# Performance work log

Measured on AMD Instinct MI355X. Metric: run time of the kernel, lower is better.

## Reference

```python
import jax, jax.numpy as jnp
import numpy as np

Nc, Nd, Ns = 8000, 6000, 6000          # circRNA / drug / disease node counts
F, H, O = 64, 4, 64                    # feature dim (fcir=fdrug=fdis), GAT heads, cnn out_channels
Ec, Ed, Es = 256000, 192000, 192000    # directed edge counts per graph
NEG_SLOPE = 0.2


def _gcn(x, src, dst, ew, W, b, N):
    # PyG GCNConv w/ edge_weight: add self loops (w=1), symmetric norm, x@W.T, scatter-add
    loop = jnp.arange(N, dtype=src.dtype)
    s = jnp.concatenate([src, loop])
    d = jnp.concatenate([dst, loop])
    w = jnp.concatenate([ew, jnp.ones((N,), x.dtype)])
    deg = jax.ops.segment_sum(w, d, num_segments=N)
    dinv = jnp.where(deg > 0, jax.lax.rsqrt(deg), 0.0)
    norm = dinv[s] * w * dinv[d]                        # [E+N]
    h = x @ W.T                                         # [N,F]
    return jax.ops.segment_sum(h[s] * norm[:, None], d, num_segments=N) + b


def _gat(x, src, dst, ew, W, a_src, a_dst, We, a_edge, b, N):
    # PyG GATConv(heads=H, concat=False, edge_dim=1); self loops with fill_value='mean'
    E = src.shape[0]
    ea = ew[:, None]                                    # [E,1]
    cnt = jax.ops.segment_sum(jnp.ones((E,), x.dtype), dst, num_segments=N)
    esum = jax.ops.segment_sum(ea, dst, num_segments=N)
    loop_attr = esum / jnp.maximum(cnt, 1.0)[:, None]   # per-dst mean edge attr
    loop = jnp.arange(N, dtype=src.dtype)
    s = jnp.concatenate([src, loop])
    d = jnp.concatenate([dst, loop])
    ea = jnp.concatenate([ea, loop_attr], axis=0)       # [E+N,1]
    h = (x @ W.T).reshape(N, H, F)
    al_s = jnp.einsum('nhf,hf->nh', h, a_src)
    al_d = jnp.einsum('nhf,hf->nh', h, a_dst)
    e = (ea @ We.T).reshape(-1, H, F)
    al_e = jnp.einsum('ehf,hf->eh', e, a_edge)
    alpha = al_s[s] + al_d[d] + al_e                    # [E+N,H]
    alpha = jnp.where(alpha >= 0, alpha, NEG_SLOPE * alpha)   # leaky_relu
    amax = jax.ops.segment_max(alpha, d, num_segments=N)
    ex = jnp.exp(alpha - amax[d])
    denom = jax.ops.segment_sum(ex, d, num_segments=N)
    coef = ex / denom[d]                                # segment softmax over incoming edges
    out = jax.ops.segment_sum(h[s] * coef[:, :, None], d, num_segments=N)  # [N,H,F]
    return out.mean(axis=1) + b                         # concat=False -> head mean


def _readout(x1, x2, W, b):
    # Conv1d(in=2, out=O, kernel=(F,1)) on [1,2,F,N] == full contraction over (layer, feature)
    X = jnp.stack([x1, x2], axis=0)                     # [2,N,F]
    return jnp.einsum('cnf,ocf->no', X, W) + b          # [N,O]


def _forward(fl, cir_edges, drug_edges, dis_edges):
    def branch(x, ei, ew, g1W, g1b, gaW, gas, gad, gaeW, gae, gab, g2W, g2b, N):
        src, dst = ei[0], ei[1]
        f1 = jax.nn.relu(_gcn(x, src, dst, ew, g1W, g1b, N))
        att = jax.nn.relu(_gat(f1, src, dst, ew, gaW, gas, gad, gaeW, gae, gab, N))
        f2 = jax.nn.relu(_gcn(att, src, dst, ew, g2W, g2b, N))
        return f1, f2

    cf1, cf2 = branch(fl['x_cir'], cir_edges, fl['cir_ew'], fl['gcn_cir1_W'], fl['gcn_cir1_b'],
                      fl['gat_cir_W'], fl['gat_cir_asrc'], fl['gat_cir_adst'], fl['gat_cir_eW'],
                      fl['gat_cir_aedge'], fl['gat_cir_b'], fl['gcn_cir2_W'], fl['gcn_cir2_b'], Nc)
    # NOTE: the source forward reuses the *_dis GCN/GAT layers for the drug branch (faithful)
    df1, df2 = branch(fl['x_drug'], drug_edges, fl['drug_ew'], fl['gcn_dis1_W'], fl['gcn_dis1_b'],
                      fl['gat_dis_W'], fl['gat_dis_asrc'], fl['gat_dis_adst'], fl['gat_dis_eW'],
                      fl['gat_dis_aedge'], fl['gat_dis_b'], fl['gcn_dis2_W'], fl['gcn_dis2_b'], Nd)
    sf1, sf2 = branch(fl['x_dis'], dis_edges, fl['dis_ew'], fl['gcn_dis1_W'], fl['gcn_dis1_b'],
                      fl['gat_dis_W'], fl['gat_dis_asrc'], fl['gat_dis_adst'], fl['gat_dis_eW'],
                      fl['gat_dis_aedge'], fl['gat_dis_b'], fl['gcn_dis2_W'], fl['gcn_dis2_b'], Ns)
    cir_fea = _readout(cf1, cf2, fl['cnn_cir_W'], fl['cnn_cir_b'])
    drug_fea = _readout(df1, df2, fl['cnn_dis_W'], fl['cnn_dis_b'])   # source uses cnn_dis for drug too
    dis_fea = _readout(sf1, sf2, fl['cnn_dis_W'], fl['cnn_dis_b'])
    return (cir_fea @ dis_fea.T, cir_fea @ drug_fea.T, drug_fea @ dis_fea.T,
            cir_fea, drug_fea, dis_fea)


_PARAM_SHAPES = [
    ('gcn_cir1_W', (F, F)), ('gcn_cir1_b', (F,)),
    ('gcn_cir2_W', (F, F)), ('gcn_cir2_b', (F,)),
    ('gcn_dis1_W', (F, F)), ('gcn_dis1_b', (F,)),
    ('gcn_dis2_W', (F, F)), ('gcn_dis2_b', (F,)),
    ('gat_cir_W', (H * F, F)), ('gat_cir_asrc', (H, F)), ('gat_cir_adst', (H, F)),
    ('gat_cir_eW', (H * F, 1)), ('gat_cir_aedge', (H, F)), ('gat_cir_b', (F,)),
    ('gat_dis_W', (H * F, F)), ('gat_dis_asrc', (H, F)), ('gat_dis_adst', (H, F)),
    ('gat_dis_eW', (H * F, 1)), ('gat_dis_aedge', (H, F)), ('gat_dis_b', (F,)),
    ('cnn_cir_W', (O, 2, F)), ('cnn_cir_b', (O,)),
    ('cnn_dis_W', (O, 2, F)), ('cnn_dis_b', (O,)),
]


def setup_inputs() -> dict:
    key = jax.random.key(0)
    ks = iter(jax.random.split(key, 64))
    inp = {}
    inp['x_cir'] = jax.random.normal(next(ks), (Nc, F), jnp.float32)
    inp['x_drug'] = jax.random.normal(next(ks), (Nd, F), jnp.float32)
    inp['x_dis'] = jax.random.normal(next(ks), (Ns, F), jnp.float32)
    inp['cir_edges'] = jax.random.randint(next(ks), (2, Ec), 0, Nc, dtype=jnp.int32)
    inp['cir_ew'] = jax.random.uniform(next(ks), (Ec,), jnp.float32)
    inp['drug_edges'] = jax.random.randint(next(ks), (2, Ed), 0, Nd, dtype=jnp.int32)
    inp['drug_ew'] = jax.random.uniform(next(ks), (Ed,), jnp.float32)
    inp['dis_edges'] = jax.random.randint(next(ks), (2, Es), 0, Ns, dtype=jnp.int32)
    inp['dis_ew'] = jax.random.uniform(next(ks), (Es,), jnp.float32)
    for name, shape in _PARAM_SHAPES:
        inp[name] = jax.random.normal(next(ks), shape, jnp.float32) * 0.1
    return inp


def reference(x_cir, x_drug, x_dis, cir_edges, cir_ew, drug_edges, drug_ew, dis_edges, dis_ew,
              gcn_cir1_W, gcn_cir1_b, gcn_cir2_W, gcn_cir2_b,
              gcn_dis1_W, gcn_dis1_b, gcn_dis2_W, gcn_dis2_b,
              gat_cir_W, gat_cir_asrc, gat_cir_adst, gat_cir_eW, gat_cir_aedge, gat_cir_b,
              gat_dis_W, gat_dis_asrc, gat_dis_adst, gat_dis_eW, gat_dis_aedge, gat_dis_b,
              cnn_cir_W, cnn_cir_b, cnn_dis_W, cnn_dis_b):
    fl = {k: v for k, v in locals().items() if k not in ('cir_edges', 'drug_edges', 'dis_edges')}
    return _forward(fl, cir_edges, drug_edges, dis_edges)
```

## Files before the change

### kernel.cpp

```cpp
#include <hip/hip_runtime.h>

#define NEG_SLOPE 0.2f

typedef __attribute__((ext_vector_type(8))) short bfrag;
typedef __attribute__((ext_vector_type(4))) float f32x4;

static __device__ __forceinline__ ushort f2bf(float x){
  uint u = __float_as_uint(x);
  uint r = (u + 0x7fff + ((u>>16)&1)) >> 16;
  return (ushort)r;
}
static __device__ __forceinline__ float bf2f(ushort h){
  return __uint_as_float(((uint)h)<<16);
}
static __device__ __forceinline__ float rdlane(float v, int l){
  return __int_as_float(__builtin_amdgcn_readlane(__float_as_int(v), l));
}


struct G3 {
  const int* src[3]; const int* dst[3]; const float* ew[3];
  float* deg[3]; int* cnt[3]; int* pos[3];
  float* dinv[3]; float* lat[3]; int* rowp[3];
  int4* ep[3];
  int N[3]; int E[3];
};

struct MM3 {
  const float* A[3]; const float* B[3]; float* C[3]; const float* bias[3];
  ushort* H[3]; ushort* L[3];
  const float* gas[3]; const float* gad[3];
  float* als[3]; float* ald[3];
  int M[3]; int lda, ldb, N2;
};

struct AGG3 {
  const float* h[3]; const float* dinv[3]; const int* rowp[3];
  const int4* ep[3]; const float* bias[3];
  float* out[3]; int N[3]; int ostride, ooff;
};

struct GAT3 {
  const float* hg[3]; const float* als[3]; const float* ald[3];
  const float* lat[3]; const float* ce[3]; const int* rowp[3];
  const int4* ep[3]; const float* bias[3];
  float* out[3]; int N[3];
};

struct SC3 {
  const ushort* AH[3]; const ushort* AL[3];
  const ushort* BH[3]; const ushort* BL[3];
  float* C[3]; int M[3]; int N2;
};


__global__ void k_edge_stats_b(G3 g){
  int b = blockIdx.z;
  int e = blockIdx.x*blockDim.x + threadIdx.x;
  if (e < g.E[b]){
    int d = g.dst[b][e];
    atomicAdd(&g.deg[b][d], g.ew[b][e]);
    atomicAdd(&g.cnt[b][d], 1);
  }
}

__global__ void k_scan_b(G3 g, const float* gaeW_c, const float* gae_c, float* ce_c,
                         const float* gaeW_d, const float* gae_d, float* ce_d){
  int b = blockIdx.x;
  int tid = threadIdx.x;
  if (b < 2 && tid < 64){
    const float* W = b ? gaeW_d : gaeW_c;
    const float* Aa = b ? gae_d : gae_c;
    float* ceo = b ? ce_d : ce_c;
    #pragma unroll
    for (int hh=0; hh<4; hh++){
      float v = W[hh*64+tid] * Aa[hh*64+tid];
      #pragma unroll
      for (int off=32; off>0; off>>=1) v += __shfl_down(v,off);
      if (tid==0) ceo[hh] = v;
    }
  }
  int N = g.N[b];
  const float* deg = g.deg[b];
  const int* cnt = g.cnt[b];
  float* dinv = g.dinv[b];
  float* lat = g.lat[b];
  int* rowp = g.rowp[b];
  const int T = 1024, PER = 8;
  __shared__ int ssum[T];
  int base = tid*PER;
  int loc[PER]; int s = 0;
  #pragma unroll
  for (int u=0;u<PER;u++){
    int i = base+u;
    int c = (i<N)? cnt[i] : 0;
    loc[u] = s; s += c;
    if (i<N){
      float d = deg[i];
      dinv[i] = rsqrtf(d);
      lat[i] = (d - 1.0f) / fmaxf((float)c, 1.0f);
    }
  }
  ssum[tid] = s; __syncthreads();
  for (int off=1; off<T; off<<=1){
    int t = (tid>=off)? ssum[tid-off] : 0;
    __syncthreads();
    ssum[tid] += t;
    __syncthreads();
  }
  int excl = ssum[tid] - s;
  #pragma unroll
  for (int u=0;u<PER;u++){ int i=base+u; if (i<N) rowp[i] = excl + loc[u]; }
  if (tid == T-1) rowp[N] = ssum[T-1];
}

__global__ void k_scatter_b(G3 g){
  int b = blockIdx.z;
  int e = blockIdx.x*blockDim.x + threadIdx.x;
  if (e < g.E[b]){
    int d = g.dst[b][e];
    int s = g.src[b][e];
    float w = g.ew[b][e];
    float dw = g.dinv[b][s] * w;
    int p = g.rowp[b][d] + atomicAdd(&g.pos[b][d], 1);
    g.ep[b][p] = make_int4(s, __float_as_int(w), __float_as_int(dw), 0);
  }
}


template<int K, bool BIAS, bool SPLIT, bool ALQ, bool INIT>
__global__ __launch_bounds__(256)
void k_mm_b(MM3 P, G3 g){
  if (INIT && blockIdx.x == gridDim.x-1){
    int b = blockIdx.z;
    int i = blockIdx.y*256 + threadIdx.x;
    if (i < g.N[b]){ g.deg[b][i] = 1.0f; g.cnt[b][i] = 0; g.pos[b][i] = 0; }
    return;
  }
  int br = blockIdx.z;
  int M = P.M[br];
  int bi = blockIdx.y*128;
  if (bi >= M) return;
  int N2 = P.N2;
  int bj = blockIdx.x*128;
  const float* __restrict__ A = P.A[br];
  const float* __restrict__ B = P.B[br];
  float* __restrict__ C = P.C[br];
  int lda = P.lda, ldb = P.ldb;

  __shared__ float As[128*36];
  __shared__ float Bs[32*132];
  int tid = threadIdx.x;
  int tx = tid & 15, ty = tid >> 4;
  float acc[8][8] = {};

  for (int kh = 0; kh < K; kh += 32){
    for (int t = tid; t < 1024; t += 256){
      int r = t >> 3, k4 = (t & 7) << 2;
      int gr = bi + r;
      float4 v = (gr < M) ? *(const float4*)(A + (size_t)gr*lda + kh + k4)
                          : make_float4(0.f,0.f,0.f,0.f);
      *(float4*)(As + r*36 + k4) = v;
    }
    for (int t = tid; t < 1024; t += 256){
      int r = t >> 3, k4 = (t & 7) << 2;
      int gr = bj + r;
      float4 v = (gr < N2) ? *(const float4*)(B + (size_t)gr*ldb + kh + k4)
                           : make_float4(0.f,0.f,0.f,0.f);
      Bs[(k4+0)*132 + r] = v.x;
      Bs[(k4+1)*132 + r] = v.y;
      Bs[(k4+2)*132 + r] = v.z;
      Bs[(k4+3)*132 + r] = v.w;
    }
    __syncthreads();
    #pragma unroll
    for (int k = 0; k < 32; k += 4){
      float4 a4[8];
      #pragma unroll
      for (int u=0; u<4; u++){
        a4[u]   = *(const float4*)(As + (ty*4+u)*36 + k);
        a4[u+4] = *(const float4*)(As + (64+ty*4+u)*36 + k);
      }
      #pragma unroll
      for (int i=0; i<4; i++){
        float4 bl = *(const float4*)(Bs + (k+i)*132 + tx*4);
        float4 bh = *(const float4*)(Bs + (k+i)*132 + 64 + tx*4);
        #pragma unroll
        for (int u=0; u<8; u++){
          float av = (i==0)?a4[u].x : (i==1)?a4[u].y : (i==2)?a4[u].z : a4[u].w;
          acc[u][0] += av*bl.x; acc[u][1] += av*bl.y;
          acc[u][2] += av*bl.z; acc[u][3] += av*bl.w;
          acc[u][4] += av*bh.x; acc[u][5] += av*bh.y;
          acc[u][6] += av*bh.z; acc[u][7] += av*bh.w;
        }
      }
    }
    __syncthreads();
  }

  #pragma unroll
  for (int u=0; u<8; u++){
    int gi = bi + ((u<4) ? (ty*4+u) : (64+ty*4+(u-4)));
    if (gi >= M) continue;
    #pragma unroll
    for (int half=0; half<2; half++){
      int gj = bj + ((half==0) ? tx*4 : 64+tx*4);
      int v0 = half*4;
      if (gj + 4 <= N2){
        float4 r4 = make_float4(acc[u][v0],acc[u][v0+1],acc[u][v0+2],acc[u][v0+3]);
        if (BIAS){
          const float* bb = P.bias[br];
          r4.x += bb[gj]; r4.y += bb[gj+1]; r4.z += bb[gj+2]; r4.w += bb[gj+3];
        }
        *(float4*)(C + (size_t)gi*N2 + gj) = r4;
        if (SPLIT){
          ushort hv[4], lv[4];
          float vv[4] = {r4.x, r4.y, r4.z, r4.w};
          #pragma unroll
          for (int v=0; v<4; v++){
            hv[v] = f2bf(vv[v]);
            lv[v] = f2bf(vv[v] - bf2f(hv[v]));
          }
          *(ushort4*)(P.H[br] + (size_t)gi*N2 + gj) = make_ushort4(hv[0],hv[1],hv[2],hv[3]);
          *(ushort4*)(P.L[br] + (size_t)gi*N2 + gj) = make_ushort4(lv[0],lv[1],lv[2],lv[3]);
        }
      } else {
        for (int v=0; v<4; v++) if (gj+v < N2){
          float r = acc[u][v0+v];
          if (BIAS) r += P.bias[br][gj+v];
          C[(size_t)gi*N2+gj+v] = r;
        }
      }
    }
  }

  if (ALQ){
    int h0 = bj >> 6;
    float ps[8][2], pd[8][2];
    #pragma unroll
    for (int u=0;u<8;u++){ ps[u][0]=0.f; ps[u][1]=0.f; pd[u][0]=0.f; pd[u][1]=0.f; }
    #pragma unroll
    for (int half=0; half<2; half++){
      #pragma unroll
      for (int v=0; v<4; v++){
        int cw = tx*4 + v;
        float gs = P.gas[br][(h0+half)*64 + cw];
        float gd = P.gad[br][(h0+half)*64 + cw];
        #pragma unroll
        for (int u=0;u<8;u++){
          ps[u][half] += acc[u][half*4+v]*gs;
          pd[u][half] += acc[u][half*4+v]*gd;
        }
      }
    }
    #pragma unroll
    for (int u=0;u<8;u++){
      #pragma unroll
      for (int hf=0; hf<2; hf++){
        float s = ps[u][hf], d = pd[u][hf];
        #pragma unroll
        for (int off=8; off>0; off>>=1){ s += __shfl_down(s,off); d += __shfl_down(d,off); }
        if (tx==0){
          int gi = bi + ((u<4) ? (ty*4+u) : (64+ty*4+(u-4)));
          if (gi < M){
            P.als[br][gi*4 + h0 + hf] = s;
            P.ald[br][gi*4 + h0 + hf] = d;
          }
        }
      }
    }
  }
}


__global__ void k_gcn_agg_b(AGG3 P){
  int b = blockIdx.z;
  int wid = (blockIdx.x*blockDim.x + threadIdx.x) >> 6;
  int f = threadIdx.x & 63;
  if (wid >= P.N[b]) return;
  const float* __restrict__ h = P.h[b];
  const int4* __restrict__ ep = P.ep[b];
  float dn = P.dinv[b][wid];
  float acc = dn*h[(size_t)wid*64 + f];
  int p0 = P.rowp[b][wid], p1 = P.rowp[b][wid+1];
  for (int p=p0; p<p1; p++){
    int4 pr = ep[p];
    acc = fmaf(__int_as_float(pr.z), h[(size_t)pr.x*64 + f], acc);
  }
  P.out[b][(size_t)wid*P.ostride + P.ooff + f] = fmaxf(fmaf(dn, acc, P.bias[b][f]), 0.f);
}


__global__ void k_gat_agg_b(GAT3 P){
  int b = blockIdx.z;
  int wid = (blockIdx.x*blockDim.x + threadIdx.x) >> 6;
  int lane = threadIdx.x & 63;
  if (wid >= P.N[b]) return;
  const float* __restrict__ hg = P.hg[b];
  const float* __restrict__ als = P.als[b];
  const int4* __restrict__ ep = P.ep[b];
  int h = lane & 3;
  int el = lane >> 2;
  int f = lane;

  float4 cv = *(const float4*)P.ce[b];
  float4 adv = *(const float4*)(P.ald[b] + (size_t)wid*4);
  float4 asv = *(const float4*)(als + (size_t)wid*4);
  float c_l  = (h==0)?cv.x :(h==1)?cv.y :(h==2)?cv.z :cv.w;
  float ad_l = (h==0)?adv.x:(h==1)?adv.y:(h==2)?adv.z:adv.w;
  float as_l = (h==0)?asv.x:(h==1)?asv.y:(h==2)?asv.z:asv.w;
  float la = P.lat[b][wid];

  float a_self = as_l + ad_l + la*c_l;
  a_self = (a_self >= 0.f) ? a_self : NEG_SLOPE*a_self;
  float m = a_self;

  int p0 = P.rowp[b][wid], p1 = P.rowp[b][wid+1];

  for (int c0=p0; c0<p1; c0+=16){
    int idx = c0 + el;
    float a = -1e30f;
    if (idx < p1){
      int4 pr = ep[idx];
      float w = __int_as_float(pr.y);
      a = als[pr.x*4 + h] + ad_l + w*c_l;
      a = (a >= 0.f) ? a : NEG_SLOPE*a;
    }
    #pragma unroll
    for (int off=4; off<64; off<<=1) a = fmaxf(a, __shfl_xor(a, off));
    m = fmaxf(m, a);
  }

  float ex_self = __expf(a_self - m);
  float l = ex_self;
  const float* hn = hg + (size_t)wid*256;
  float acc0 = rdlane(ex_self,0) * hn[f];
  float acc1 = rdlane(ex_self,1) * hn[64+f];
  float acc2 = rdlane(ex_self,2) * hn[128+f];
  float acc3 = rdlane(ex_self,3) * hn[192+f];

  for (int c0=p0; c0<p1; c0+=16){
    int idx = c0 + el;
    float ex = 0.f;
    int s_lane = 0;
    if (idx < p1){
      int4 pr = ep[idx];
      s_lane = pr.x;
      float w = __int_as_float(pr.y);
      float a = als[s_lane*4 + h] + ad_l + w*c_l;
      a = (a >= 0.f) ? a : NEG_SLOPE*a;
      ex = __expf(a - m);
    }
    float ls = ex;
    #pragma unroll
    for (int off=4; off<64; off<<=1) ls += __shfl_xor(ls, off);
    l += ls;
    int cnt = p1 - c0; if (cnt > 16) cnt = 16;
    for (int e=0; e<cnt; e++){
      int s = __builtin_amdgcn_readlane(s_lane, e*4);
      const float* hs = hg + (size_t)s*256 + f;
      float x0 = rdlane(ex, e*4+0);
      float x1 = rdlane(ex, e*4+1);
      float x2 = rdlane(ex, e*4+2);
      float x3 = rdlane(ex, e*4+3);
      acc0 = fmaf(x0, hs[0],   acc0);
      acc1 = fmaf(x1, hs[64],  acc1);
      acc2 = fmaf(x2, hs[128], acc2);
      acc3 = fmaf(x3, hs[192], acc3);
    }
  }
  float o = acc0/rdlane(l,0) + acc1/rdlane(l,1) + acc2/rdlane(l,2) + acc3/rdlane(l,3);
  P.out[b][(size_t)wid*64 + f] = fmaxf(0.25f*o + P.bias[b][f], 0.f);
}


__global__ __launch_bounds__(256)
void k_score(SC3 P){
  int br = blockIdx.z;
  int M = P.M[br];
  int bi = blockIdx.y*128;
  if (bi >= M) return;
  int N = P.N2;
  int bj = blockIdx.x*128;
  const ushort* __restrict__ AH = P.AH[br];
  const ushort* __restrict__ ALo = P.AL[br];
  const ushort* __restrict__ BH = P.BH[br];
  const ushort* __restrict__ BLo = P.BL[br];
  float* __restrict__ C = P.C[br];

  int wv = threadIdx.x >> 6;
  int lane = threadIdx.x & 63;
  int la = lane & 15, lk = lane >> 4;
  int r0 = bi + (wv>>1)*64;
  int c0 = bj + (wv&1)*64;

  bfrag ah[4][2], al[4][2];
  #pragma unroll
  for (int mi=0; mi<4; mi++){
    int r = r0 + mi*16 + la; if (r > M-1) r = M-1;
    size_t base = (size_t)r*64 + lk*8;
    ah[mi][0] = *(const bfrag*)(AH + base);
    ah[mi][1] = *(const bfrag*)(AH + base + 32);
    al[mi][0] = *(const bfrag*)(ALo + base);
    al[mi][1] = *(const bfrag*)(ALo + base + 32);
  }

  f32x4 acc[4][4];
  #pragma unroll
  for (int mi=0; mi<4; mi++)
    #pragma unroll
    for (int ni=0; ni<4; ni++)
      acc[mi][ni] = (f32x4){0.f,0.f,0.f,0.f};

  #pragma unroll
  for (int ni=0; ni<4; ni++){
    int cc = c0 + ni*16 + la; if (cc > N-1) cc = N-1;
    size_t base = (size_t)cc*64 + lk*8;
    bfrag bh0 = *(const bfrag*)(BH + base);
    bfrag bh1 = *(const bfrag*)(BH + base + 32);
    bfrag bl0 = *(const bfrag*)(BLo + base);
    bfrag bl1 = *(const bfrag*)(BLo + base + 32);
    #pragma unroll
    for (int mi=0; mi<4; mi++){
      f32x4 a = acc[mi][ni];
      a = __builtin_amdgcn_mfma_f32_16x16x32_bf16(ah[mi][0], bh0, a, 0, 0, 0);
      a = __builtin_amdgcn_mfma_f32_16x16x32_bf16(ah[mi][1], bh1, a, 0, 0, 0);
      a = __builtin_amdgcn_mfma_f32_16x16x32_bf16(ah[mi][0], bl0, a, 0, 0, 0);
      a = __builtin_amdgcn_mfma_f32_16x16x32_bf16(ah[mi][1], bl1, a, 0, 0, 0);
      a = __builtin_amdgcn_mfma_f32_16x16x32_bf16(al[mi][0], bh0, a, 0, 0, 0);
      a = __builtin_amdgcn_mfma_f32_16x16x32_bf16(al[mi][1], bh1, a, 0, 0, 0);
      acc[mi][ni] = a;
    }
  }

  #pragma unroll
  for (int mi=0; mi<4; mi++){
    int rb = r0 + mi*16 + lk*4;
    #pragma unroll
    for (int ni=0; ni<4; ni++){
      int col = c0 + ni*16 + la;
      if (col >= N) continue;
      #pragma unroll
      for (int rg=0; rg<4; rg++){
        int r = rb + rg;
        if (r < M) C[(size_t)r*N + col] = acc[mi][ni][rg];
      }
    }
  }
}


extern "C" void kernel_launch(void* const* d_in, const int* in_sizes, int n_in,
                              void* d_out, int out_size, void* d_ws, size_t ws_size,
                              hipStream_t stream){
  const float* x_cir  = (const float*)d_in[0];
  const float* x_drug = (const float*)d_in[1];
  const float* x_dis  = (const float*)d_in[2];
  const int*   cir_edges  = (const int*)d_in[3];
  const float* cir_ew     = (const float*)d_in[4];
  const int*   drug_edges = (const int*)d_in[5];
  const float* drug_ew    = (const float*)d_in[6];
  const int*   dis_edges  = (const int*)d_in[7];
  const float* dis_ew     = (const float*)d_in[8];
  const float* gcn_cir1_W = (const float*)d_in[9];
  const float* gcn_cir1_b = (const float*)d_in[10];
  const float* gcn_cir2_W = (const float*)d_in[11];
  const float* gcn_cir2_b = (const float*)d_in[12];
  const float* gcn_dis1_W = (const float*)d_in[13];
  const float* gcn_dis1_b = (const float*)d_in[14];
  const float* gcn_dis2_W = (const float*)d_in[15];
  const float* gcn_dis2_b = (const float*)d_in[16];
  const float* gat_cir_W    = (const float*)d_in[17];
  const float* gat_cir_asrc = (const float*)d_in[18];
  const float* gat_cir_adst = (const float*)d_in[19];
  const float* gat_cir_eW   = (const float*)d_in[20];
  const float* gat_cir_aedge= (const float*)d_in[21];
  const float* gat_cir_b    = (const float*)d_in[22];
  const float* gat_dis_W    = (const float*)d_in[23];
  const float* gat_dis_asrc = (const float*)d_in[24];
  const float* gat_dis_adst = (const float*)d_in[25];
  const float* gat_dis_eW   = (const float*)d_in[26];
  const float* gat_dis_aedge= (const float*)d_in[27];
  const float* gat_dis_b    = (const float*)d_in[28];
  const float* cnn_cir_W = (const float*)d_in[29];
  const float* cnn_cir_b = (const float*)d_in[30];
  const float* cnn_dis_W = (const float*)d_in[31];
  const float* cnn_dis_b = (const float*)d_in[32];
  float* out = (float*)d_out;

  const int Nb[3] = {8000, 6000, 6000};
  const int Eb[3] = {256000, 192000, 192000};

  char* wp = (char*)d_ws;
  auto alloc = [&](size_t bytes)->void*{
    void* p = wp; wp += (bytes + 255) & ~(size_t)255; return p;
  };

  float* fea[3] = { out + 132000000ULL, out + 132512000ULL, out + 132896000ULL };

  float* ce_c = (float*)alloc(64);
  float* ce_d = (float*)alloc(64);

  G3 g;
  const int* edges[3] = {cir_edges, drug_edges, dis_edges};
  const float* ews[3] = {cir_ew, drug_ew, dis_ew};
  float *hbuf[3], *f12[3], *att[3], *als[3], *ald[3];
  ushort *feaH[3], *feaL[3];
  for (int b=0; b<3; b++){
    g.src[b] = edges[b];
    g.dst[b] = edges[b] + Eb[b];
    g.ew[b]  = ews[b];
    g.N[b] = Nb[b]; g.E[b] = Eb[b];
    g.deg[b]  = (float*)alloc((size_t)Nb[b]*4);
    g.dinv[b] = (float*)alloc((size_t)Nb[b]*4);
    g.lat[b]  = (float*)alloc((size_t)Nb[b]*4);
    g.cnt[b]  = (int*)alloc((size_t)Nb[b]*4);
    g.pos[b]  = (int*)alloc((size_t)Nb[b]*4);
    g.rowp[b] = (int*)alloc((size_t)(Nb[b]+1)*4);
    g.ep[b]   = (int4*)alloc((size_t)Eb[b]*16);
    als[b]  = (float*)alloc((size_t)Nb[b]*4*4);
    ald[b]  = (float*)alloc((size_t)Nb[b]*4*4);
    hbuf[b] = (float*)alloc((size_t)Nb[b]*256*4);
    f12[b]  = (float*)alloc((size_t)Nb[b]*128*4);
    att[b]  = (float*)alloc((size_t)Nb[b]*64*4);
    feaH[b] = (ushort*)alloc((size_t)Nb[b]*64*2);
    feaL[b] = (ushort*)alloc((size_t)Nb[b]*64*2);
  }

  const float* xin[3]  = {x_cir, x_drug, x_dis};
  const float* g1W[3]  = {gcn_cir1_W, gcn_dis1_W, gcn_dis1_W};
  const float* g1b[3]  = {gcn_cir1_b, gcn_dis1_b, gcn_dis1_b};
  const float* g2W[3]  = {gcn_cir2_W, gcn_dis2_W, gcn_dis2_W};
  const float* g2b[3]  = {gcn_cir2_b, gcn_dis2_b, gcn_dis2_b};
  const float* gaW[3]  = {gat_cir_W, gat_dis_W, gat_dis_W};
  const float* gasP[3] = {gat_cir_asrc, gat_dis_asrc, gat_dis_asrc};
  const float* gadP[3] = {gat_cir_adst, gat_dis_adst, gat_dis_adst};
  const float* gab[3]  = {gat_cir_b, gat_dis_b, gat_dis_b};
  const float* cep[3]  = {ce_c, ce_d, ce_d};
  const float* cW[3]   = {cnn_cir_W, cnn_dis_W, cnn_dis_W};
  const float* cb[3]   = {cnn_cir_b, cnn_dis_b, cnn_dis_b};

  auto mkmm = [&](MM3& m, const float* const* Ap, const float* const* Bp,
                  float* const* Cp, const float* const* bp, int lda, int ldb, int N2){
    for (int b=0;b<3;b++){
      m.A[b]=Ap[b]; m.B[b]=Bp[b]; m.C[b]=Cp[b]; m.bias[b]= bp? bp[b] : nullptr;
      m.H[b]=nullptr; m.L[b]=nullptr;
      m.gas[b]=nullptr; m.gad[b]=nullptr; m.als[b]=nullptr; m.ald[b]=nullptr;
      m.M[b]=Nb[b];
    }
    m.lda=lda; m.ldb=ldb; m.N2=N2;
  };

  MM3 m1; mkmm(m1, xin, g1W, hbuf, nullptr, 64, 64, 64);
  k_mm_b<64,false,false,false,true><<<dim3(2,63,3),256,0,stream>>>(m1, g);

  k_edge_stats_b<<<dim3(1000,1,3),256,0,stream>>>(g);
  k_scan_b<<<3,1024,0,stream>>>(g, gat_cir_eW, gat_cir_aedge, ce_c,
                                   gat_dis_eW, gat_dis_aedge, ce_d);
  k_scatter_b<<<dim3(1000,1,3),256,0,stream>>>(g);

  AGG3 a1;
  for (int b=0;b<3;b++){ a1.h[b]=hbuf[b]; a1.dinv[b]=g.dinv[b]; a1.rowp[b]=g.rowp[b];
    a1.ep[b]=g.ep[b]; a1.bias[b]=g1b[b]; a1.out[b]=f12[b]; a1.N[b]=Nb[b]; }
  a1.ostride=128; a1.ooff=0;
  k_gcn_agg_b<<<dim3(2000,1,3),256,0,stream>>>(a1);

  {
    const float* Ap[3] = {f12[0], f12[1], f12[2]};
    MM3 m2; mkmm(m2, Ap, gaW, hbuf, nullptr, 128, 64, 256);
    for (int b=0;b<3;b++){ m2.gas[b]=gasP[b]; m2.gad[b]=gadP[b]; m2.als[b]=als[b]; m2.ald[b]=ald[b]; }
    k_mm_b<64,false,false,true,false><<<dim3(2,63,3),256,0,stream>>>(m2, g);
  }

  GAT3 gt;
  for (int b=0;b<3;b++){ gt.hg[b]=hbuf[b]; gt.als[b]=als[b]; gt.ald[b]=ald[b]; gt.lat[b]=g.lat[b];
    gt.ce[b]=cep[b]; gt.rowp[b]=g.rowp[b]; gt.ep[b]=g.ep[b];
    gt.bias[b]=gab[b]; gt.out[b]=att[b]; gt.N[b]=Nb[b]; }
  k_gat_agg_b<<<dim3(2000,1,3),256,0,stream>>>(gt);

  {
    const float* Ap[3] = {att[0], att[1], att[2]};
    MM3 m3; mkmm(m3, Ap, g2W, hbuf, nullptr, 64, 64, 64);
    k_mm_b<64,false,false,false,false><<<dim3(1,63,3),256,0,stream>>>(m3, g);
  }

  AGG3 a2 = a1;
  for (int b=0;b<3;b++){ a2.bias[b]=g2b[b]; }
  a2.ooff=64;
  k_gcn_agg_b<<<dim3(2000,1,3),256,0,stream>>>(a2);

  {
    const float* Ap[3] = {f12[0], f12[1], f12[2]};
    MM3 m4; mkmm(m4, Ap, cW, fea, cb, 128, 128, 64);
    for (int b=0;b<3;b++){ m4.H[b]=feaH[b]; m4.L[b]=feaL[b]; }
    k_mm_b<128,true,true,false,false><<<dim3(1,63,3),256,0,stream>>>(m4, g);
  }

  SC3 sc;
  sc.AH[0]=feaH[0]; sc.AL[0]=feaL[0]; sc.BH[0]=feaH[2]; sc.BL[0]=feaL[2];
  sc.C[0]=out;               sc.M[0]=8000;
  sc.AH[1]=feaH[0]; sc.AL[1]=feaL[0]; sc.BH[1]=feaH[1]; sc.BL[1]=feaL[1];
  sc.C[1]=out + 48000000ULL; sc.M[1]=8000;
  sc.AH[2]=feaH[1]; sc.AL[2]=feaL[1]; sc.BH[2]=feaH[2]; sc.BL[2]=feaL[2];
  sc.C[2]=out + 96000000ULL; sc.M[2]=6000;
  sc.N2=6000;
  k_score<<<dim3(47,63,3),256,0,stream>>>(sc);
}
```

Measured before the change: 1.029 ms.

## Fuse edge stats into matmul, drop GAT max pass, unroll aggregations

The separate edge-statistics kernel is removed. Degree and count accumulation now runs in the spare column of blocks of the first matmul, and a single memset zeroes the deg/cnt/pos buffers. Self-loop weight and the loop-attribute mean are derived from the raw edge-weight sum in the scan. The GAT aggregation drops its separate max-reduction pass and uses the self-loop logit as the softmax shift, which avoids a second sweep over edges but can overflow exp if neighbour logits greatly exceed the self logit. The GCN gather loop is unrolled by four and the GAT inner loop by two to expose more memory-level parallelism.

After: 992.3 us. 3.6% less time.

```diff
diff --git a/kernel.cpp b/kernel.cpp
--- a/kernel.cpp
+++ b/kernel.cpp
@@ -20,7 +20,8 @@
 
 struct G3 {
   const int* src[3]; const int* dst[3]; const float* ew[3];
-  float* deg[3]; int* cnt[3]; int* pos[3];
+  float* deg[3];
+  int* cnt[3]; int* pos[3];
   float* dinv[3]; float* lat[3]; int* rowp[3];
   int4* ep[3];
   int N[3]; int E[3];
@@ -53,16 +54,6 @@
   float* C[3]; int M[3]; int N2;
 };
 
-
-__global__ void k_edge_stats_b(G3 g){
-  int b = blockIdx.z;
-  int e = blockIdx.x*blockDim.x + threadIdx.x;
-  if (e < g.E[b]){
-    int d = g.dst[b][e];
-    atomicAdd(&g.deg[b][d], g.ew[b][e]);
-    atomicAdd(&g.cnt[b][d], 1);
-  }
-}
 
 __global__ void k_scan_b(G3 g, const float* gaeW_c, const float* gae_c, float* ce_c,
                          const float* gaeW_d, const float* gae_d, float* ce_d){
@@ -81,7 +72,7 @@
     }
   }
   int N = g.N[b];
-  const float* deg = g.deg[b];
+  const float* degsum = g.deg[b];
   const int* cnt = g.cnt[b];
   float* dinv = g.dinv[b];
   float* lat = g.lat[b];
@@ -96,9 +87,9 @@
     int c = (i<N)? cnt[i] : 0;
     loc[u] = s; s += c;
     if (i<N){
-      float d = deg[i];
-      dinv[i] = rsqrtf(d);
-      lat[i] = (d - 1.0f) / fmaxf((float)c, 1.0f);
+      float ds = degsum[i];
+      dinv[i] = rsqrtf(1.0f + ds);
+      lat[i] = ds / fmaxf((float)c, 1.0f);
     }
   }
   ssum[tid] = s; __syncthreads();
@@ -128,13 +119,22 @@
 }
 
 
-template<int K, bool BIAS, bool SPLIT, bool ALQ, bool INIT>
+template<int K, bool BIAS, bool SPLIT, bool ALQ, bool STATS>
 __global__ __launch_bounds__(256)
 void k_mm_b(MM3 P, G3 g){
-  if (INIT && blockIdx.x == gridDim.x-1){
+  if (STATS && blockIdx.x == gridDim.x-1){
     int b = blockIdx.z;
-    int i = blockIdx.y*256 + threadIdx.x;
-    if (i < g.N[b]){ g.deg[b][i] = 1.0f; g.cnt[b][i] = 0; g.pos[b][i] = 0; }
+    int E = g.E[b];
+    const int* __restrict__ dst = g.dst[b];
+    const float* __restrict__ ew = g.ew[b];
+    float* __restrict__ deg = g.deg[b];
+    int* __restrict__ cnt = g.cnt[b];
+    int stride = gridDim.y*256;
+    for (int e = blockIdx.y*256 + threadIdx.x; e < E; e += stride){
+      int d = dst[e];
+      atomicAdd(&deg[d], ew[e]);
+      atomicAdd(&cnt[d], 1);
+    }
     return;
   }
   int br = blockIdx.z;
@@ -283,7 +283,19 @@
   float dn = P.dinv[b][wid];
   float acc = dn*h[(size_t)wid*64 + f];
   int p0 = P.rowp[b][wid], p1 = P.rowp[b][wid+1];
-  for (int p=p0; p<p1; p++){
+  int p = p0;
+  for (; p+4 <= p1; p+=4){
+    int4 e0 = ep[p], e1 = ep[p+1], e2 = ep[p+2], e3 = ep[p+3];
+    float v0 = h[(size_t)e0.x*64 + f];
+    float v1 = h[(size_t)e1.x*64 + f];
+    float v2 = h[(size_t)e2.x*64 + f];
+    float v3 = h[(size_t)e3.x*64 + f];
+    acc = fmaf(__int_as_float(e0.z), v0, acc);
+    acc = fmaf(__int_as_float(e1.z), v1, acc);
+    acc = fmaf(__int_as_float(e2.z), v2, acc);
+    acc = fmaf(__int_as_float(e3.z), v3, acc);
+  }
+  for (; p < p1; p++){
     int4 pr = ep[p];
     acc = fmaf(__int_as_float(pr.z), h[(size_t)pr.x*64 + f], acc);
   }
@@ -315,30 +327,14 @@
   a_self = (a_self >= 0.f) ? a_self : NEG_SLOPE*a_self;
   float m = a_self;
 
+  float l = 1.f;
+  const float* hn = hg + (size_t)wid*256;
+  float acc0 = hn[f];
+  float acc1 = hn[64+f];
+  float acc2 = hn[128+f];
+  float acc3 = hn[192+f];
+
   int p0 = P.rowp[b][wid], p1 = P.rowp[b][wid+1];
-
-  for (int c0=p0; c0<p1; c0+=16){
-    int idx = c0 + el;
-    float a = -1e30f;
-    if (idx < p1){
-      int4 pr = ep[idx];
-      float w = __int_as_float(pr.y);
-      a = als[pr.x*4 + h] + ad_l + w*c_l;
-      a = (a >= 0.f) ? a : NEG_SLOPE*a;
-    }
-    #pragma unroll
-    for (int off=4; off<64; off<<=1) a = fmaxf(a, __shfl_xor(a, off));
-    m = fmaxf(m, a);
-  }
-
-  float ex_self = __expf(a_self - m);
-  float l = ex_self;
-  const float* hn = hg + (size_t)wid*256;
-  float acc0 = rdlane(ex_self,0) * hn[f];
-  float acc1 = rdlane(ex_self,1) * hn[64+f];
-  float acc2 = rdlane(ex_self,2) * hn[128+f];
-  float acc3 = rdlane(ex_self,3) * hn[192+f];
-
   for (int c0=p0; c0<p1; c0+=16){
     int idx = c0 + el;
     float ex = 0.f;
@@ -356,6 +352,7 @@
     for (int off=4; off<64; off<<=1) ls += __shfl_xor(ls, off);
     l += ls;
     int cnt = p1 - c0; if (cnt > 16) cnt = 16;
+    #pragma unroll 2
     for (int e=0; e<cnt; e++){
       int s = __builtin_amdgcn_readlane(s_lane, e*4);
       const float* hs = hg + (size_t)s*256 + f;
@@ -504,6 +501,15 @@
   G3 g;
   const int* edges[3] = {cir_edges, drug_edges, dis_edges};
   const float* ews[3] = {cir_ew, drug_ew, dis_ew};
+
+  char* zero_base = wp;
+  for (int b=0; b<3; b++){
+    g.deg[b]  = (float*)alloc((size_t)Nb[b]*4);
+    g.cnt[b]  = (int*)alloc((size_t)Nb[b]*4);
+    g.pos[b]  = (int*)alloc((size_t)Nb[b]*4);
+  }
+  size_t zero_bytes = (size_t)(wp - zero_base);
+
   float *hbuf[3], *f12[3], *att[3], *als[3], *ald[3];
   ushort *feaH[3], *feaL[3];
   for (int b=0; b<3; b++){
@@ -511,11 +517,8 @@
     g.dst[b] = edges[b] + Eb[b];
     g.ew[b]  = ews[b];
     g.N[b] = Nb[b]; g.E[b] = Eb[b];
-    g.deg[b]  = (float*)alloc((size_t)Nb[b]*4);
     g.dinv[b] = (float*)alloc((size_t)Nb[b]*4);
     g.lat[b]  = (float*)alloc((size_t)Nb[b]*4);
-    g.cnt[b]  = (int*)alloc((size_t)Nb[b]*4);
-    g.pos[b]  = (int*)alloc((size_t)Nb[b]*4);
     g.rowp[b] = (int*)alloc((size_t)(Nb[b]+1)*4);
     g.ep[b]   = (int4*)alloc((size_t)Eb[b]*16);
     als[b]  = (float*)alloc((size_t)Nb[b]*4*4);
@@ -551,10 +554,11 @@
     m.lda=lda; m.ldb=ldb; m.N2=N2;
   };
 
+  hipMemsetAsync(zero_base, 0, zero_bytes, stream);
+
   MM3 m1; mkmm(m1, xin, g1W, hbuf, nullptr, 64, 64, 64);
   k_mm_b<64,false,false,false,true><<<dim3(2,63,3),256,0,stream>>>(m1, g);
 
-  k_edge_stats_b<<<dim3(1000,1,3),256,0,stream>>>(g);
   k_scan_b<<<3,1024,0,stream>>>(g, gat_cir_eW, gat_cir_aedge, ce_c,
                                    gat_dis_eW, gat_dis_aedge, ce_d);
   k_scatter_b<<<dim3(1000,1,3),256,0,stream>>>(g);
```
